# Kernel optimization log

Hardware: AMD Instinct MI355X
Metric: run time of the kernel (lower is better)

## Reference

```python
import math
import jax, jax.numpy as jnp
import numpy as np

# ---- static config ----
B, S, HID = 2, 8192, 1024
H, D = 8, 128                      # num_heads, head_dim = hidden // heads
CHUNK = 128                        # attention_chunk_size
PAST = 128 - 1                     # attention_context_left - 1
FUT = 128                          # attention_context_right
CTX = CHUNK + PAST + FUT           # 383
POS = CTX + 1                      # relative position table length (rel_shift pads to CTX+1)
CAP = 50.0                         # attention_logit_cap
Q_SCALE = D ** (-0.5) / math.log(2.0)
K_SCALE = math.log1p(math.e) / math.log(2.0)
NB = S // CHUNK                    # 64 blocks (S divisible by chunk -> no tail padding)


def setup_inputs() -> dict:
    key = jax.random.key(0)
    ks = jax.random.split(key, 8)
    s = 0.02
    return {
        "hidden_states": jax.random.normal(ks[0], (B, S, HID), jnp.float32),
        "position_embeddings": jax.random.normal(ks[1], (POS, HID), jnp.float32),
        "Wq": jax.random.normal(ks[2], (HID, H * D), jnp.float32) * s,
        "Wk": jax.random.normal(ks[3], (HID, H * D), jnp.float32) * s,
        "Wv": jax.random.normal(ks[4], (HID, H * D), jnp.float32) * s,
        "Wrel": jax.random.normal(ks[5], (HID, H * D), jnp.float32) * s,
        "Wpost": jax.random.normal(ks[6], (HID, HID), jnp.float32) * s,
        "per_dim_scale": jax.random.normal(ks[7], (D,), jnp.float32) * 0.1,
    }


def reference(hidden_states, position_embeddings, Wq, Wk, Wv, Wrel, Wpost, per_dim_scale):
    # projections (clipped-linear clamps are +/-inf -> no-ops); bias-free linears
    q = (hidden_states @ Wq).reshape(B, S, H, D)
    k = (hidden_states @ Wk).reshape(B, S, H, D)
    v = (hidden_states @ Wv).reshape(B, S, H, D)

    q = q * (Q_SCALE * jax.nn.softplus(per_dim_scale))  # per-dim scaling fused into q
    k = k * K_SCALE

    # _convert_to_block: [B, NB, CHUNK, H, D] (S % CHUNK == 0 -> no pad)
    qb = q.reshape(B, NB, CHUNK, H, D)

    # _extract_block_context: pad (PAST, FUT + CHUNK - 1) then unfold window=CTX step=CHUNK
    pad = ((0, 0), (PAST, FUT + CHUNK - 1), (0, 0), (0, 0))
    kp = jnp.pad(k, pad)
    vp = jnp.pad(v, pad)
    idx = jnp.arange(NB)[:, None] * CHUNK + jnp.arange(CTX)[None, :]  # [NB, CTX]
    kc = kp[:, idx]  # [B, NB, CTX, H, D]
    vc = vp[:, idx]  # [B, NB, CTX, H, D]

    # relative keys: [POS, H, D]
    rel_k = (position_embeddings @ Wrel).reshape(POS, H, D)

    # content scores: [B, H, NB, CHUNK, CTX]
    ac = jnp.einsum('bnchd,bnkhd->bhnck', qb, kc)
    # position scores before shift: [B, H, NB, CHUNK, POS]
    bd = jnp.einsum('bnchd,phd->bhncp', qb, rel_k)
    # Transformer-XL rel_shift (POS == CTX+1 so pad amount is zero)
    bd = bd.reshape(B, H, NB, CHUNK * POS)[..., : CHUNK * CTX]
    bd = bd.reshape(B, H, NB, CHUNK, CTX)

    # tanh soft-cap + softmax (no attention_mask)
    logits = jnp.tanh((ac + bd) / CAP) * CAP
    attn = jax.nn.softmax(logits, axis=-1)

    # weighted values -> [B, NB, CHUNK, H, D] -> [B, S, HID]
    out = jnp.einsum('bhnck,bnkhd->bnchd', attn, vc).reshape(B, S, H * D)
    return out @ Wpost
```

## Files before the change

### kernel.cpp

```cpp
#include <hip/hip_runtime.h>
#include <cmath>


using bf16x8 = __attribute__((ext_vector_type(8))) short;
using f32x4  = __attribute__((ext_vector_type(4))) float;
using s16x4  = __attribute__((ext_vector_type(4))) short;

__device__ __forceinline__ short f2bf(float f) {
  unsigned u = __float_as_uint(f);
  u = (u + 0x7FFF + ((u >> 16) & 1)) >> 16;
  return (short)u;
}
__device__ __forceinline__ float bf2f(unsigned short s) {
  return __uint_as_float(((unsigned)s) << 16);
}

__device__ __forceinline__ void gl16(void* lds, const void* gptr) {
  __builtin_amdgcn_global_load_lds(
      (const __attribute__((address_space(1))) unsigned int*)gptr,
      (__attribute__((address_space(3))) unsigned int*)lds, 16, 0, 0);
}

__global__ void cvt_bf16_k(const float* __restrict__ in, short* __restrict__ out, int n) {
  int i = (blockIdx.x * 256 + threadIdx.x) * 4;
  if (i + 3 < n) {
    float4 v = *(const float4*)&in[i];
    s16x4 o;
    o[0] = f2bf(v.x); o[1] = f2bf(v.y); o[2] = f2bf(v.z); o[3] = f2bf(v.w);
    *(s16x4*)&out[i] = o;
  }
}

__global__ void wtrans_k(const float* __restrict__ W, short* __restrict__ Wt) {
  __shared__ float T[64 * 65];
  const int tid = threadIdx.x;
  const int bx = blockIdx.x, by = blockIdx.y;
#pragma unroll
  for (int it = 0; it < 4; ++it) {
    int ci = it * 256 + tid;
    int k = ci >> 4, n4 = (ci & 15) * 4;
    float4 v = *(const float4*)&W[(size_t)(by * 64 + k) * 1024 + bx * 64 + n4];
    T[k * 65 + n4 + 0] = v.x;
    T[k * 65 + n4 + 1] = v.y;
    T[k * 65 + n4 + 2] = v.z;
    T[k * 65 + n4 + 3] = v.w;
  }
  __syncthreads();
#pragma unroll
  for (int it = 0; it < 2; ++it) {
    int co = it * 256 + tid;
    int nn = co >> 3, k8 = (co & 7) * 8;
    bf16x8 o;
#pragma unroll
    for (int jj = 0; jj < 8; ++jj) o[jj] = f2bf(T[(k8 + jj) * 65 + nn]);
    *(bf16x8*)&Wt[(size_t)(bx * 64 + nn) * 1024 + by * 64 + k8] = o;
  }
}

__global__ void qscale_k(const float* __restrict__ pds, float* __restrict__ qs, double qsb) {
  int d = threadIdx.x;
  double x = (double)pds[d];
  qs[d] = (float)(qsb * log1p(exp(x)));
}

__global__ void vpadzero_k(short* __restrict__ vpadT) {
  int row = blockIdx.x;
  int t = threadIdx.x;
  int key = (t < 127) ? t : (8192 + t);
  vpadT[(size_t)row * 8448 + key] = 0;
}

__global__ __launch_bounds__(256, 3)
void qkv_fused_k(const short* __restrict__ A, const short* __restrict__ Bt3,
                 short* __restrict__ q_bf, short* __restrict__ kpad,
                 short* __restrict__ vpadT,
                 const float* __restrict__ qsc, float kscale) {
  __shared__ __align__(16) short As[128 * 32];
  __shared__ __align__(16) short Bs[128 * 32];
  __shared__ __align__(16) short Tv[128 * 136];

  const int tid = threadIdx.x;
  const int lane = tid & 63, wid = tid >> 6;
  const int q4 = lane >> 4, l16 = lane & 15;
  const int wr = wid >> 1, wc = wid & 1;

  const int id = blockIdx.x;
  const int xcd = id & 7, local = id >> 3;
  const int mm = local / 24, nn = local - mm * 24;
  const int m0 = (xcd * 16 + mm) * 128;
  const int w = nn >> 3, nc = nn & 7;
  const short* Bt = Bt3 + ((size_t)w * 1024 + nc * 128) * 1024;

  const f32x4 z4 = {0.f, 0.f, 0.f, 0.f};
  f32x4 acc[4][4];
#pragma unroll
  for (int i = 0; i < 4; ++i)
#pragma unroll
    for (int j = 0; j < 4; ++j) acc[i][j] = z4;

  const int r0 = tid >> 2, s0_ = (tid & 3) * 8;

  for (int kk = 0; kk < 1024; kk += 32) {
    __syncthreads();
    gl16(&As[tid * 8],         A  + (size_t)(m0 + r0) * 1024 + kk + s0_);
    gl16(&Bs[tid * 8],         Bt + (size_t)r0 * 1024 + kk + s0_);
    gl16(&As[(256 + tid) * 8], A  + (size_t)(m0 + 64 + r0) * 1024 + kk + s0_);
    gl16(&Bs[(256 + tid) * 8], Bt + (size_t)(64 + r0) * 1024 + kk + s0_);
    __syncthreads();
    bf16x8 af[4], bfv[4];
#pragma unroll
    for (int i = 0; i < 4; ++i)
      af[i] = *(const bf16x8*)&As[(wr * 64 + i * 16 + l16) * 32 + q4 * 8];
#pragma unroll
    for (int j = 0; j < 4; ++j)
      bfv[j] = *(const bf16x8*)&Bs[(wc * 64 + j * 16 + l16) * 32 + q4 * 8];
#pragma unroll
    for (int i = 0; i < 4; ++i)
#pragma unroll
      for (int j = 0; j < 4; ++j)
        acc[i][j] = __builtin_amdgcn_mfma_f32_16x16x32_bf16(af[i], bfv[j], acc[i][j], 0, 0, 0);
  }

  float qsv[4];
  if (w == 0) {
#pragma unroll
    for (int j = 0; j < 4; ++j) qsv[j] = qsc[wc * 64 + j * 16 + l16];
  }

#pragma unroll
  for (int i = 0; i < 4; ++i) {
#pragma unroll
    for (int j = 0; j < 4; ++j) {
#pragma unroll
      for (int rg = 0; rg < 4; ++rg) {
        const int row = m0 + wr * 64 + i * 16 + q4 * 4 + rg;
        const int d = wc * 64 + j * 16 + l16;
        const int h = nc;
        const float v = acc[i][j][rg];
        if (w == 0) {
          int b = row >> 13, s = row & 8191;
          int n = s >> 7, c = s & 127;
          q_bf[((size_t)(((b * 64 + n) * 8 + h) * 128 + c)) * 128 + d] = f2bf(v * qsv[j]);
        } else if (w == 1) {
          int b = row >> 13, s = row & 8191;
          kpad[((size_t)(b * 8 + h) * 8448 + 127 + s) * 128 + d] = f2bf(v * kscale);
        } else {
          int sl = wr * 64 + i * 16 + q4 * 4 + rg;
          Tv[d * 136 + sl] = f2bf(v);
        }
      }
    }
  }

  if (w == 2) {
    __syncthreads();
    const int b = m0 >> 13, ss = m0 & 8191, h = nc;
#pragma unroll
    for (int it = 0; it < 8; ++it) {
      int co = it * 256 + tid;
      int d = co >> 4, s8 = (co & 15) * 8;
      *(bf16x8*)&vpadT[((size_t)(b * 8 + h) * 128 + d) * 8448 + 127 + ss + s8] =
          *(const bf16x8*)&Tv[d * 136 + s8];
    }
  }
}

__global__ __launch_bounds__(256, 3)
void post_gemm_k(const short* __restrict__ A, const short* __restrict__ Bt,
                 float* __restrict__ outf) {
  __shared__ __align__(16) short As[128 * 32];
  __shared__ __align__(16) short Bs[128 * 32];

  const int tid = threadIdx.x;
  const int lane = tid & 63, wid = tid >> 6;
  const int q4 = lane >> 4, l16 = lane & 15;
  const int wr = wid >> 1, wc = wid & 1;

  const int id = blockIdx.x;
  const int xcd = id & 7, local = id >> 3;
  const int mm = local >> 3, nn = local & 7;
  const int m0 = (xcd * 16 + mm) * 128, n0 = nn * 128;

  const f32x4 z4 = {0.f, 0.f, 0.f, 0.f};
  f32x4 acc[4][4];
#pragma unroll
  for (int i = 0; i < 4; ++i)
#pragma unroll
    for (int j = 0; j < 4; ++j) acc[i][j] = z4;

  const int r0 = tid >> 2, s0_ = (tid & 3) * 8;

  for (int kk = 0; kk < 1024; kk += 32) {
    __syncthreads();
    gl16(&As[tid * 8],         A  + (size_t)(m0 + r0) * 1024 + kk + s0_);
    gl16(&Bs[tid * 8],         Bt + (size_t)(n0 + r0) * 1024 + kk + s0_);
    gl16(&As[(256 + tid) * 8], A  + (size_t)(m0 + 64 + r0) * 1024 + kk + s0_);
    gl16(&Bs[(256 + tid) * 8], Bt + (size_t)(n0 + 64 + r0) * 1024 + kk + s0_);
    __syncthreads();
    bf16x8 af[4], bfv[4];
#pragma unroll
    for (int i = 0; i < 4; ++i)
      af[i] = *(const bf16x8*)&As[(wr * 64 + i * 16 + l16) * 32 + q4 * 8];
#pragma unroll
    for (int j = 0; j < 4; ++j)
      bfv[j] = *(const bf16x8*)&Bs[(wc * 64 + j * 16 + l16) * 32 + q4 * 8];
#pragma unroll
    for (int i = 0; i < 4; ++i)
#pragma unroll
      for (int j = 0; j < 4; ++j)
        acc[i][j] = __builtin_amdgcn_mfma_f32_16x16x32_bf16(af[i], bfv[j], acc[i][j], 0, 0, 0);
  }

#pragma unroll
  for (int i = 0; i < 4; ++i)
#pragma unroll
    for (int j = 0; j < 4; ++j)
#pragma unroll
      for (int rg = 0; rg < 4; ++rg) {
        const int row = m0 + wr * 64 + i * 16 + q4 * 4 + rg;
        const int col = n0 + wc * 64 + j * 16 + l16;
        outf[(size_t)row * 1024 + col] = acc[i][j][rg];
      }
}

__global__ __launch_bounds__(256, 2)
void rel_gemm_k(const short* __restrict__ A, const short* __restrict__ Bt,
                short* __restrict__ relk) {
  __shared__ __align__(16) short As[128 * 32];
  __shared__ __align__(16) short Bs[128 * 32];

  const int tid = threadIdx.x;
  const int lane = tid & 63, wid = tid >> 6;
  const int q4 = lane >> 4, l16 = lane & 15;
  const int wr = wid >> 1, wc = wid & 1;
  const int m0 = blockIdx.x * 128, n0 = blockIdx.y * 128;

  const f32x4 z4 = {0.f, 0.f, 0.f, 0.f};
  f32x4 acc[4][4];
#pragma unroll
  for (int i = 0; i < 4; ++i)
#pragma unroll
    for (int j = 0; j < 4; ++j) acc[i][j] = z4;

  const int r0 = tid >> 2, s0_ = (tid & 3) * 8;
  for (int kk = 0; kk < 1024; kk += 32) {
    __syncthreads();
    gl16(&As[tid * 8],         A  + (size_t)(m0 + r0) * 1024 + kk + s0_);
    gl16(&Bs[tid * 8],         Bt + (size_t)(n0 + r0) * 1024 + kk + s0_);
    gl16(&As[(256 + tid) * 8], A  + (size_t)(m0 + 64 + r0) * 1024 + kk + s0_);
    gl16(&Bs[(256 + tid) * 8], Bt + (size_t)(n0 + 64 + r0) * 1024 + kk + s0_);
    __syncthreads();
    bf16x8 af[4], bfv[4];
#pragma unroll
    for (int i = 0; i < 4; ++i)
      af[i] = *(const bf16x8*)&As[(wr * 64 + i * 16 + l16) * 32 + q4 * 8];
#pragma unroll
    for (int j = 0; j < 4; ++j)
      bfv[j] = *(const bf16x8*)&Bs[(wc * 64 + j * 16 + l16) * 32 + q4 * 8];
#pragma unroll
    for (int i = 0; i < 4; ++i)
#pragma unroll
      for (int j = 0; j < 4; ++j)
        acc[i][j] = __builtin_amdgcn_mfma_f32_16x16x32_bf16(af[i], bfv[j], acc[i][j], 0, 0, 0);
  }

#pragma unroll
  for (int i = 0; i < 4; ++i)
#pragma unroll
    for (int j = 0; j < 4; ++j)
#pragma unroll
      for (int rg = 0; rg < 4; ++rg) {
        const int row = m0 + wr * 64 + i * 16 + q4 * 4 + rg;
        const int col = n0 + wc * 64 + j * 16 + l16;
        int h = col >> 7, d = col & 127;
        relk[(size_t)(h * 384 + row) * 128 + d] = f2bf(acc[i][j][rg]);
      }
}

__global__ __launch_bounds__(256, 2)
void bd_gemm_k(const short* __restrict__ qb_b, const short* __restrict__ relk,
               short* __restrict__ bds) {
  __shared__ __align__(16) short As[128 * 32];
  __shared__ __align__(16) short Bs[128 * 32];
  const int tid = threadIdx.x;
  const int lane = tid & 63, wid = tid >> 6;
  const int q4 = lane >> 4, l16 = lane & 15;
  const int wr = wid >> 1, wc = wid & 1;
  const int p0 = blockIdx.x * 128;
  const int nh = blockIdx.y;
  const int h = nh & 7;
  const short* A = qb_b + (size_t)nh * 16384;
  const short* Bt = relk + (size_t)h * (384 * 128);
  short* bdo = bds + (size_t)nh * 49152;

  const f32x4 z4 = {0.f, 0.f, 0.f, 0.f};
  f32x4 acc[4][4];
#pragma unroll
  for (int i = 0; i < 4; ++i)
#pragma unroll
    for (int j = 0; j < 4; ++j) acc[i][j] = z4;

  const int r0 = tid >> 2, s0_ = (tid & 3) * 8;
  for (int kk = 0; kk < 128; kk += 32) {
    __syncthreads();
    gl16(&As[tid * 8],         A  + (size_t)r0 * 128 + kk + s0_);
    gl16(&Bs[tid * 8],         Bt + (size_t)(p0 + r0) * 128 + kk + s0_);
    gl16(&As[(256 + tid) * 8], A  + (size_t)(64 + r0) * 128 + kk + s0_);
    gl16(&Bs[(256 + tid) * 8], Bt + (size_t)(p0 + 64 + r0) * 128 + kk + s0_);
    __syncthreads();
    bf16x8 af[4], bfv[4];
#pragma unroll
    for (int i = 0; i < 4; ++i)
      af[i] = *(const bf16x8*)&As[(wr * 64 + i * 16 + l16) * 32 + q4 * 8];
#pragma unroll
    for (int j = 0; j < 4; ++j)
      bfv[j] = *(const bf16x8*)&Bs[(wc * 64 + j * 16 + l16) * 32 + q4 * 8];
#pragma unroll
    for (int i = 0; i < 4; ++i)
#pragma unroll
      for (int j = 0; j < 4; ++j)
        acc[i][j] = __builtin_amdgcn_mfma_f32_16x16x32_bf16(af[i], bfv[j], acc[i][j], 0, 0, 0);
  }

#pragma unroll
  for (int i = 0; i < 4; ++i)
#pragma unroll
    for (int j = 0; j < 4; ++j)
#pragma unroll
      for (int rg = 0; rg < 4; ++rg) {
        int r = wr * 64 + i * 16 + q4 * 4 + rg;
        int p = p0 + wc * 64 + j * 16 + l16;
        int t = r + p;
        int c = (t < 383) ? r : (r + 1);
        int k = (t < 383) ? t : (t - 383);
        if (c < 128) {
          int tt = k >> 7, jj = (k >> 4) & 7, ll = k & 15;
          int wa = c >> 5, ia = (c >> 4) & 1, qa = (c >> 2) & 3, ra = c & 3;
          bdo[((((size_t)tt * 8 + jj) * 256) + wa * 64 + qa * 16 + ll) * 8 + ia * 4 + ra] =
              f2bf(acc[i][j][rg]);
        }
      }
}

__global__ __launch_bounds__(256, 3)
void attn_k(const short* __restrict__ qb_b, const short* __restrict__ kpad,
            const short* __restrict__ vpadT, const short* __restrict__ bds,
            short* __restrict__ attnout, int b) {
  __shared__ __align__(16) short Ks[4 * 128 * 32];
  __shared__ __align__(16) short Ps[64 * 136];

  const int tid = threadIdx.x;
  const int lane = tid & 63, wid = tid >> 6;
  const int q4 = lane >> 4, l16 = lane & 15;
  const int bx = blockIdx.x;
  const int qh = bx & 1, nh = bx >> 1;
  const int n = nh >> 3, h = nh & 7;

  const short* qtile = qb_b + (size_t)nh * 16384 + qh * 64 * 128;
  const short* kbase = kpad + ((size_t)(b * 8 + h) * 8448 + n * 128) * 128;
  const short* vtb = vpadT + (size_t)(b * 8 + h) * 128 * 8448 + n * 128;
  const short* bdb = bds + (size_t)nh * 49152;

#pragma unroll
  for (int it = 0; it < 4; ++it) {
    int ci = it * 256 + tid;
    int dc = ci >> 8, rr = (ci >> 2) & 63, sub = (ci & 3) * 8;
    gl16(&Ks[ci * 8], qtile + rr * 128 + dc * 32 + sub);
  }
  __syncthreads();
  bf16x8 qf[4];
#pragma unroll
  for (int dc = 0; dc < 4; ++dc)
    qf[dc] = *(const bf16x8*)&Ks[dc * 2048 + (wid * 16 + l16) * 32 + q4 * 8];

  const f32x4 z4 = {0.f, 0.f, 0.f, 0.f};
  f32x4 acco[8];
#pragma unroll
  for (int j = 0; j < 8; ++j) acco[j] = z4;
  float rsum[4] = {};

  for (int t = 0; t < 3; ++t) {
    __syncthreads();
#pragma unroll
    for (int it = 0; it < 8; ++it) {
      int ci = it * 256 + tid;
      int dc = ci >> 9, rr = (ci >> 2) & 127, sub = (ci & 3) * 8;
      gl16(&Ks[ci * 8], kbase + (size_t)(t * 128 + rr) * 128 + dc * 32 + sub);
    }

    s16x4 bdv[8];
#pragma unroll
    for (int j = 0; j < 8; ++j)
      bdv[j] = *(const s16x4*)&bdb[((((size_t)t * 8 + j) * 256) +
                 (qh * 2 + (wid >> 1)) * 64 + q4 * 16 + l16) * 8 + (wid & 1) * 4];

    __syncthreads();

    f32x4 accs[8];
#pragma unroll
    for (int j = 0; j < 8; ++j) accs[j] = z4;
#pragma unroll
    for (int dc = 0; dc < 4; ++dc) {
      bf16x8 kf[8];
#pragma unroll
      for (int j = 0; j < 8; ++j)
        kf[j] = *(const bf16x8*)&Ks[dc * 4096 + (j * 16 + l16) * 32 + q4 * 8];
#pragma unroll
      for (int j = 0; j < 8; ++j)
        accs[j] = __builtin_amdgcn_mfma_f32_16x16x32_bf16(qf[dc], kf[j], accs[j], 0, 0, 0);
    }

#pragma unroll
    for (int j = 0; j < 8; ++j) {
      const int kg = t * 128 + j * 16 + l16;
#pragma unroll
      for (int rg = 0; rg < 4; ++rg) {
        float sv = accs[j][rg] + bf2f((unsigned short)bdv[j][rg]);
        float tt = exp2f(sv * 0.057707801635558534f);
        float wgt = exp2f(-144.26950408889634f * __fdividef(1.0f, tt + 1.0f));
        wgt = (kg < 383) ? wgt : 0.0f;
        accs[j][rg] = wgt;
        rsum[rg] += wgt;
      }
    }
    __syncthreads();

#pragma unroll
    for (int it = 0; it < 8; ++it) {
      int ci = it * 256 + tid;
      int kc = ci >> 9, dd = (ci >> 2) & 127, sub = (ci & 3) * 8;
      gl16(&Ks[ci * 8], vtb + (size_t)dd * 8448 + t * 128 + kc * 32 + sub);
    }
#pragma unroll
    for (int j = 0; j < 8; ++j)
#pragma unroll
      for (int rg = 0; rg < 4; ++rg) {
        int c = wid * 16 + q4 * 4 + rg;
        int kl = j * 16 + l16;
        Ps[c * 136 + kl] = f2bf(accs[j][rg]);
      }
    __syncthreads();

#pragma unroll
    for (int kc = 0; kc < 4; ++kc) {
      bf16x8 pf, vf[8];
      pf = *(const bf16x8*)&Ps[(wid * 16 + l16) * 136 + kc * 32 + q4 * 8];
#pragma unroll
      for (int j = 0; j < 8; ++j)
        vf[j] = *(const bf16x8*)&Ks[kc * 4096 + (j * 16 + l16) * 32 + q4 * 8];
#pragma unroll
      for (int j = 0; j < 8; ++j)
        acco[j] = __builtin_amdgcn_mfma_f32_16x16x32_bf16(pf, vf[j], acco[j], 0, 0, 0);
    }
  }

  float rinv[4];
#pragma unroll
  for (int rg = 0; rg < 4; ++rg) {
    float rs = rsum[rg];
    rs += __shfl_xor(rs, 1);
    rs += __shfl_xor(rs, 2);
    rs += __shfl_xor(rs, 4);
    rs += __shfl_xor(rs, 8);
    rinv[rg] = __fdividef(1.0f, rs);
  }
#pragma unroll
  for (int j = 0; j < 8; ++j)
#pragma unroll
    for (int rg = 0; rg < 4; ++rg) {
      int srow = n * 128 + qh * 64 + wid * 16 + q4 * 4 + rg;
      int col = h * 128 + j * 16 + l16;
      attnout[((size_t)b * 8192 + srow) * 1024 + col] = f2bf(acco[j][rg] * rinv[rg]);
    }
}

extern "C" void kernel_launch(void* const* d_in, const int* in_sizes, int n_in,
                              void* d_out, int out_size, void* d_ws, size_t ws_size,
                              hipStream_t stream) {
  (void)in_sizes; (void)n_in; (void)out_size; (void)ws_size;
  const float* hs    = (const float*)d_in[0];
  const float* pemb  = (const float*)d_in[1];
  const float* Wq    = (const float*)d_in[2];
  const float* Wk    = (const float*)d_in[3];
  const float* Wv    = (const float*)d_in[4];
  const float* Wrel  = (const float*)d_in[5];
  const float* Wpost = (const float*)d_in[6];
  const float* pds   = (const float*)d_in[7];
  float* out = (float*)d_out;

  char* w = (char*)d_ws;
  auto alloc = [&](size_t bytes) -> char* {
    char* p = w; w += (bytes + 255) & ~(size_t)255; return p;
  };
  short* hs_bf   = (short*)alloc((size_t)16384 * 1024 * 2);
  short* pos_bf  = (short*)alloc((size_t)384 * 1024 * 2);
  short* Wq_t    = (short*)alloc((size_t)1024 * 1024 * 2);
  short* Wk_t    = (short*)alloc((size_t)1024 * 1024 * 2);
  short* Wv_t    = (short*)alloc((size_t)1024 * 1024 * 2);
  short* Wrel_t  = (short*)alloc((size_t)1024 * 1024 * 2);
  short* Wpost_t = (short*)alloc((size_t)1024 * 1024 * 2);
  float* qsc     = (float*)alloc(512);
  short* q_bf    = (short*)alloc((size_t)2 * 64 * 8 * 128 * 128 * 2);
  short* kpad    = (short*)alloc((size_t)2 * 8 * 8448 * 128 * 2);
  short* vpadT   = (short*)alloc((size_t)2 * 8 * 128 * 8448 * 2);
  short* relk    = (short*)alloc((size_t)8 * 384 * 128 * 2);
  short* bds     = (short*)alloc((size_t)64 * 8 * 128 * 384 * 2);
  short* attnout = hs_bf;

  const float kscale = (float)(log1p(exp(1.0)) / log(2.0));
  const double qsb = (1.0 / sqrt(128.0)) / log(2.0);

  cvt_bf16_k<<<16384, 256, 0, stream>>>(hs, hs_bf, 16384 * 1024);
  cvt_bf16_k<<<384, 256, 0, stream>>>(pemb, pos_bf, 384 * 1024);
  dim3 tg(16, 16);
  wtrans_k<<<tg, 256, 0, stream>>>(Wq, Wq_t);
  wtrans_k<<<tg, 256, 0, stream>>>(Wk, Wk_t);
  wtrans_k<<<tg, 256, 0, stream>>>(Wv, Wv_t);
  wtrans_k<<<tg, 256, 0, stream>>>(Wrel, Wrel_t);
  wtrans_k<<<tg, 256, 0, stream>>>(Wpost, Wpost_t);
  qscale_k<<<1, 128, 0, stream>>>(pds, qsc, qsb);
  hipMemsetAsync(kpad, 0, (size_t)2 * 8 * 8448 * 128 * 2, stream);
  vpadzero_k<<<2048, 256, 0, stream>>>(vpadT);

  qkv_fused_k<<<3072, 256, 0, stream>>>(hs_bf, Wq_t, q_bf, kpad, vpadT, qsc, kscale);
  rel_gemm_k<<<dim3(3, 8), 256, 0, stream>>>(pos_bf, Wrel_t, relk);

  for (int b = 0; b < 2; ++b) {
    const short* qb_b = q_bf + (size_t)b * 64 * 8 * 128 * 128;
    bd_gemm_k<<<dim3(3, 512), 256, 0, stream>>>(qb_b, relk, bds);
    attn_k<<<1024, 256, 0, stream>>>(qb_b, kpad, vpadT, bds, attnout, b);
  }

  post_gemm_k<<<1024, 256, 0, stream>>>(attnout, Wpost_t, out);
}
```

Before: 554.1 us.

## Replace QKV GEMM with 256x256 tiled, double-buffered, swizzled-LDS pipelined kernel

Rewrites the fused QKV projection to use 256x256 output tiles with 512 threads, a 64-wide K step and double-buffered LDS staged through global_load_lds with an XOR swizzle. Loads for the next K tiles are interleaved with the MFMA phases, using explicit waitcnt, barriers and setprio. The aim is more data reuse per byte loaded and latency hiding that the old single-buffered 128x128 kernel lacked. In exchange it uses much more LDS and registers, which lowers occupancy, and the epilogue, including the V transpose through LDS, is reworked.

After: 544.2 us. No clear change (-1.8%).

```diff
diff --git a/kernel.cpp b/kernel.cpp
--- a/kernel.cpp
+++ b/kernel.cpp
@@ -70,97 +70,197 @@
   vpadT[(size_t)row * 8448 + key] = 0;
 }
 
-__global__ __launch_bounds__(256, 3)
-void qkv_fused_k(const short* __restrict__ A, const short* __restrict__ Bt3,
-                 short* __restrict__ q_bf, short* __restrict__ kpad,
-                 short* __restrict__ vpadT,
-                 const float* __restrict__ qsc, float kscale) {
-  __shared__ __align__(16) short As[128 * 32];
-  __shared__ __align__(16) short Bs[128 * 32];
-  __shared__ __align__(16) short Tv[128 * 136];
+
+__device__ __forceinline__ void stage_half(short* ldsb, const short* gbase, int tid) {
+#pragma unroll
+  for (int it = 0; it < 2; ++it) {
+    int L = (it * 512 + tid) * 16;
+    int r = L >> 7;
+    int cb = (L & 127) ^ (((L >> 9) & 1) << 5);
+    gl16((char*)ldsb + L, gbase + (size_t)r * 1024 + (cb >> 1));
+  }
+}
+
+__device__ __forceinline__ bf16x8 frag_ld(const short* hb, int row, int ks, int q4) {
+  int cb = (ks * 64 + q4 * 16) ^ (((row >> 2) & 1) << 5);
+  return *(const bf16x8*)((const char*)hb + row * 128 + cb);
+}
+
+__global__ __launch_bounds__(512, 2)
+void qkv256_k(const short* __restrict__ A, const short* __restrict__ Bt3,
+              short* __restrict__ q_bf, short* __restrict__ kpad,
+              short* __restrict__ vpadT,
+              const float* __restrict__ qsc, float kscale) {
+  __shared__ __align__(16) short lds[65536];
 
   const int tid = threadIdx.x;
   const int lane = tid & 63, wid = tid >> 6;
   const int q4 = lane >> 4, l16 = lane & 15;
-  const int wr = wid >> 1, wc = wid & 1;
+  const int wr = wid >> 2, wc = wid & 3;
 
   const int id = blockIdx.x;
   const int xcd = id & 7, local = id >> 3;
-  const int mm = local / 24, nn = local - mm * 24;
-  const int m0 = (xcd * 16 + mm) * 128;
-  const int w = nn >> 3, nc = nn & 7;
-  const short* Bt = Bt3 + ((size_t)w * 1024 + nc * 128) * 1024;
+  const int mm = xcd * 8 + local / 12, nn = local % 12;
+  const int m0 = mm * 256, n0 = nn * 256;
+
+  const short* Abase = A + (size_t)m0 * 1024;
+  const short* Bbase = Bt3 + (size_t)n0 * 1024;
 
   const f32x4 z4 = {0.f, 0.f, 0.f, 0.f};
-  f32x4 acc[4][4];
-#pragma unroll
-  for (int i = 0; i < 4; ++i)
+  f32x4 acc[8][4];
+#pragma unroll
+  for (int i = 0; i < 8; ++i)
 #pragma unroll
     for (int j = 0; j < 4; ++j) acc[i][j] = z4;
 
-  const int r0 = tid >> 2, s0_ = (tid & 3) * 8;
-
-  for (int kk = 0; kk < 1024; kk += 32) {
-    __syncthreads();
-    gl16(&As[tid * 8],         A  + (size_t)(m0 + r0) * 1024 + kk + s0_);
-    gl16(&Bs[tid * 8],         Bt + (size_t)r0 * 1024 + kk + s0_);
-    gl16(&As[(256 + tid) * 8], A  + (size_t)(m0 + 64 + r0) * 1024 + kk + s0_);
-    gl16(&Bs[(256 + tid) * 8], Bt + (size_t)(64 + r0) * 1024 + kk + s0_);
-    __syncthreads();
-    bf16x8 af[4], bfv[4];
-#pragma unroll
-    for (int i = 0; i < 4; ++i)
-      af[i] = *(const bf16x8*)&As[(wr * 64 + i * 16 + l16) * 32 + q4 * 8];
-#pragma unroll
-    for (int j = 0; j < 4; ++j)
-      bfv[j] = *(const bf16x8*)&Bs[(wc * 64 + j * 16 + l16) * 32 + q4 * 8];
-#pragma unroll
-    for (int i = 0; i < 4; ++i)
+  stage_half(lds + 0 * 32768 + 0 * 8192, Abase, tid);
+  stage_half(lds + 0 * 32768 + 1 * 8192, Abase + 128 * 1024, tid);
+  stage_half(lds + 0 * 32768 + 2 * 8192, Bbase, tid);
+  stage_half(lds + 0 * 32768 + 3 * 8192, Bbase + 128 * 1024, tid);
+  stage_half(lds + 1 * 32768 + 2 * 8192, Bbase + 64, tid);
+  stage_half(lds + 1 * 32768 + 3 * 8192, Bbase + 128 * 1024 + 64, tid);
+  asm volatile("s_waitcnt vmcnt(4)" ::: "memory");
+  __builtin_amdgcn_s_barrier();
+
+  for (int kt = 0; kt < 16; ++kt) {
+    const int buf = kt & 1;
+    const short* Acur = lds + buf * 32768 + wr * 8192;
+    const short* Bcur = lds + buf * 32768 + (2 + (wc >> 1)) * 8192;
+    const int brow0 = (wc & 1) * 64;
+
+    bf16x8 bfr[4][2];
+
+    {
 #pragma unroll
       for (int j = 0; j < 4; ++j)
-        acc[i][j] = __builtin_amdgcn_mfma_f32_16x16x32_bf16(af[i], bfv[j], acc[i][j], 0, 0, 0);
-  }
-
-  float qsv[4];
+#pragma unroll
+        for (int ks = 0; ks < 2; ++ks)
+          bfr[j][ks] = frag_ld(Bcur, brow0 + j * 16 + l16, ks, q4);
+      bf16x8 afr[2][2];
+#pragma unroll
+      for (int m2 = 0; m2 < 2; ++m2)
+#pragma unroll
+        for (int ks = 0; ks < 2; ++ks)
+          afr[m2][ks] = frag_ld(Acur, m2 * 16 + l16, ks, q4);
+      if (kt < 15)
+        stage_half(lds + (buf ^ 1) * 32768 + 0 * 8192, Abase + (size_t)(kt + 1) * 64, tid);
+      asm volatile("s_waitcnt lgkmcnt(8)" ::: "memory");
+      __builtin_amdgcn_s_barrier();
+      asm volatile("s_waitcnt lgkmcnt(0)" ::: "memory");
+      __builtin_amdgcn_s_setprio(1);
+#pragma unroll
+      for (int ks = 0; ks < 2; ++ks)
+#pragma unroll
+        for (int m2 = 0; m2 < 2; ++m2)
+#pragma unroll
+          for (int j = 0; j < 4; ++j)
+            acc[m2][j] = __builtin_amdgcn_mfma_f32_16x16x32_bf16(
+                afr[m2][ks], bfr[j][ks], acc[m2][j], 0, 0, 0);
+      __builtin_amdgcn_s_setprio(0);
+      __builtin_amdgcn_s_barrier();
+    }
+
+#pragma unroll
+    for (int p = 1; p < 4; ++p) {
+      bf16x8 afr[2][2];
+#pragma unroll
+      for (int m2 = 0; m2 < 2; ++m2)
+#pragma unroll
+        for (int ks = 0; ks < 2; ++ks)
+          afr[m2][ks] = frag_ld(Acur, (p * 2 + m2) * 16 + l16, ks, q4);
+      if (p == 1) {
+        if (kt < 15)
+          stage_half(lds + (buf ^ 1) * 32768 + 1 * 8192,
+                     Abase + 128 * 1024 + (size_t)(kt + 1) * 64, tid);
+      } else if (p == 2) {
+        if (kt < 14)
+          stage_half(lds + buf * 32768 + 2 * 8192, Bbase + (size_t)(kt + 2) * 64, tid);
+      } else {
+        if (kt < 14)
+          stage_half(lds + buf * 32768 + 3 * 8192,
+                     Bbase + 128 * 1024 + (size_t)(kt + 2) * 64, tid);
+      }
+      __builtin_amdgcn_s_barrier();
+      asm volatile("s_waitcnt lgkmcnt(0)" ::: "memory");
+      __builtin_amdgcn_s_setprio(1);
+#pragma unroll
+      for (int ks = 0; ks < 2; ++ks)
+#pragma unroll
+        for (int m2 = 0; m2 < 2; ++m2)
+#pragma unroll
+          for (int j = 0; j < 4; ++j)
+            acc[p * 2 + m2][j] = __builtin_amdgcn_mfma_f32_16x16x32_bf16(
+                afr[m2][ks], bfr[j][ks], acc[p * 2 + m2][j], 0, 0, 0);
+      __builtin_amdgcn_s_setprio(0);
+      if (p == 3) {
+        if (kt < 14) asm volatile("s_waitcnt vmcnt(4)" ::: "memory");
+        else         asm volatile("s_waitcnt vmcnt(0)" ::: "memory");
+      }
+      __builtin_amdgcn_s_barrier();
+    }
+  }
+
+  const int w = n0 >> 10;
+  const int cw = n0 & 1023;
+  const int b = m0 >> 13;
+  const int s_base = (m0 & 8191) + wr * 128;
+
   if (w == 0) {
-#pragma unroll
-    for (int j = 0; j < 4; ++j) qsv[j] = qsc[wc * 64 + j * 16 + l16];
-  }
-
-#pragma unroll
-  for (int i = 0; i < 4; ++i) {
-#pragma unroll
-    for (int j = 0; j < 4; ++j) {
-#pragma unroll
-      for (int rg = 0; rg < 4; ++rg) {
-        const int row = m0 + wr * 64 + i * 16 + q4 * 4 + rg;
-        const int d = wc * 64 + j * 16 + l16;
-        const int h = nc;
-        const float v = acc[i][j][rg];
-        if (w == 0) {
-          int b = row >> 13, s = row & 8191;
+    float qsv[4];
+#pragma unroll
+    for (int j = 0; j < 4; ++j) qsv[j] = qsc[(cw + wc * 64 + j * 16 + l16) & 127];
+#pragma unroll
+    for (int m = 0; m < 8; ++m)
+#pragma unroll
+      for (int j = 0; j < 4; ++j)
+#pragma unroll
+        for (int rg = 0; rg < 4; ++rg) {
+          int s = s_base + m * 16 + q4 * 4 + rg;
+          int col = cw + wc * 64 + j * 16 + l16;
+          int h = col >> 7, d = col & 127;
           int n = s >> 7, c = s & 127;
-          q_bf[((size_t)(((b * 64 + n) * 8 + h) * 128 + c)) * 128 + d] = f2bf(v * qsv[j]);
-        } else if (w == 1) {
-          int b = row >> 13, s = row & 8191;
-          kpad[((size_t)(b * 8 + h) * 8448 + 127 + s) * 128 + d] = f2bf(v * kscale);
-        } else {
-          int sl = wr * 64 + i * 16 + q4 * 4 + rg;
-          Tv[d * 136 + sl] = f2bf(v);
+          q_bf[((size_t)(((b * 64 + n) * 8 + h) * 128 + c)) * 128 + d] =
+              f2bf(acc[m][j][rg] * qsv[j]);
         }
-      }
-    }
-  }
-
-  if (w == 2) {
-    __syncthreads();
-    const int b = m0 >> 13, ss = m0 & 8191, h = nc;
-#pragma unroll
-    for (int it = 0; it < 8; ++it) {
-      int co = it * 256 + tid;
-      int d = co >> 4, s8 = (co & 15) * 8;
-      *(bf16x8*)&vpadT[((size_t)(b * 8 + h) * 128 + d) * 8448 + 127 + ss + s8] =
-          *(const bf16x8*)&Tv[d * 136 + s8];
+  } else if (w == 1) {
+#pragma unroll
+    for (int m = 0; m < 8; ++m)
+#pragma unroll
+      for (int j = 0; j < 4; ++j)
+#pragma unroll
+        for (int rg = 0; rg < 4; ++rg) {
+          int s = s_base + m * 16 + q4 * 4 + rg;
+          int col = cw + wc * 64 + j * 16 + l16;
+          int h = col >> 7, d = col & 127;
+          kpad[((size_t)(b * 8 + h) * 8448 + 127 + s) * 128 + d] =
+              f2bf(acc[m][j][rg] * kscale);
+        }
+  } else {
+    short* T = lds;
+#pragma unroll
+    for (int hh = 0; hh < 2; ++hh) {
+      __syncthreads();
+      if ((wc >> 1) == hh) {
+#pragma unroll
+        for (int m = 0; m < 8; ++m)
+#pragma unroll
+          for (int j = 0; j < 4; ++j)
+#pragma unroll
+            for (int rg = 0; rg < 4; ++rg) {
+              int sl = wr * 128 + m * 16 + q4 * 4 + rg;
+              int dl = (wc & 1) * 64 + j * 16 + l16;
+              T[dl * 264 + sl] = f2bf(acc[m][j][rg]);
+            }
+      }
+      __syncthreads();
+      const int h = (cw >> 7) + hh;
+#pragma unroll
+      for (int it = 0; it < 8; ++it) {
+        int co = it * 512 + tid;
+        int dd = co >> 5, s8 = (co & 31) * 8;
+        *(bf16x8*)&vpadT[((size_t)(b * 8 + h) * 128 + dd) * 8448 + 127 + (m0 & 8191) + s8] =
+            *(const bf16x8*)&T[dd * 264 + s8];
+      }
     }
   }
 }
@@ -522,7 +622,7 @@
   hipMemsetAsync(kpad, 0, (size_t)2 * 8 * 8448 * 128 * 2, stream);
   vpadzero_k<<<2048, 256, 0, stream>>>(vpadT);
 
-  qkv_fused_k<<<3072, 256, 0, stream>>>(hs_bf, Wq_t, q_bf, kpad, vpadT, qsc, kscale);
+  qkv256_k<<<768, 512, 0, stream>>>(hs_bf, Wq_t, q_bf, kpad, vpadT, qsc, kscale);
   rel_gemm_k<<<dim3(3, 8), 256, 0, stream>>>(pos_bf, Wrel_t, relk);
 
   for (int b = 0; b < 2; ++b) {
```
